# Kernel optimization log

Measured on AMD Instinct MI355X. Metric: run time of the kernel, lower is better.

Reference implementation:

```python
import jax, jax.numpy as jnp
import numpy as np
import math

ATTN_C = 32
HEADS = 8
IN_C = 256
PAIR_C = 128
B, M, N = 1, 128, 256


def _layernorm(x, w, b, eps=1e-5):
    mu = jnp.mean(x, axis=-1, keepdims=True)
    xc = x - mu
    var = jnp.mean(xc * xc, axis=-1, keepdims=True)
    return xc * jax.lax.rsqrt(var + eps) * w + b


def setup_inputs() -> dict:
    key = jax.random.key(0)
    ks = jax.random.split(key, 10)
    s1 = 1.0 / math.sqrt(IN_C)
    s2 = 1.0 / math.sqrt(PAIR_C)
    s3 = 1.0 / math.sqrt(ATTN_C * HEADS)
    return {
        "x1d": jax.random.normal(ks[0], (B, M, N, IN_C), jnp.float32),
        "x2d": jax.random.normal(ks[1], (B, N, N, PAIR_C), jnp.float32),
        "norm_w": jnp.ones((IN_C,), jnp.float32),
        "norm_b": jnp.zeros((IN_C,), jnp.float32),
        "qkv_w": jax.random.normal(ks[2], (3 * ATTN_C * HEADS, IN_C), jnp.float32) * s1,
        "x2d_w": jax.random.normal(ks[3], (HEADS, PAIR_C), jnp.float32) * s2,
        "gate_w": jax.random.normal(ks[4], (ATTN_C * HEADS, IN_C), jnp.float32) * s1,
        "gate_b": jnp.zeros((ATTN_C * HEADS,), jnp.float32),
        "final_w": jax.random.normal(ks[5], (IN_C, ATTN_C * HEADS), jnp.float32) * s3,
        "final_b": jnp.zeros((IN_C,), jnp.float32),
    }


def reference(x1d, x2d, norm_w, norm_b, qkv_w, x2d_w, gate_w, gate_b, final_w, final_b):
    c, h = ATTN_C, HEADS
    x = _layernorm(x1d, norm_w, norm_b)                      # [B,M,N,IN_C]
    qkv = (x @ qkv_w.T).reshape(*x.shape[:-1], c, 3 * h)     # [B,M,N,c,3h]
    q, k, v = qkv[..., :h], qkv[..., h:2 * h], qkv[..., 2 * h:]
    aff = jnp.einsum('bmich,bmjch->bmijh', q, k)             # [B,M,N,N,H]
    gate = jax.nn.sigmoid(x @ gate_w.T + gate_b).reshape(*x.shape[:-1], c, h)
    factor = 1.0 / math.sqrt(c)
    bias = (x2d @ x2d_w.T) * factor                          # [B,N,N,H]
    weights = jax.nn.softmax(aff + bias[:, None], axis=-2)   # softmax over j
    out = jnp.einsum('bmrch,bmirh->bmich', v, weights) * gate
    out = out.reshape(*x.shape[:-1], c * h) @ final_w.T + final_b
    return out
```

## Files before the change

kernel.cpp:

```cpp
#include <hip/hip_runtime.h>
#include <math.h>

typedef short bf16x8 __attribute__((ext_vector_type(8)));
typedef float f32x4  __attribute__((ext_vector_type(4)));

#define NPOS 32768

#define OFF_CHI   0u
#define OFF_AHI   100663296u
#define OFF_ATTN  134217728u
#define OFF_BIAST 150994944u
#define OFF_WHI   153354240u
#define OFF_W2P   154402816u
#define OFF_GBP   154533888u

__device__ __forceinline__ short f2bf(float x) {
    unsigned int u = __float_as_uint(x);
    unsigned int r = (u + 0x7FFFu + ((u >> 16) & 1u)) >> 16;
    return (short)r;
}
__device__ __forceinline__ float bf2f(short s) {
    return __uint_as_float(((unsigned int)(unsigned short)s) << 16);
}
__device__ __forceinline__ void async_copy16(const void* g, void* l) {
    __builtin_amdgcn_global_load_lds(
        (const __attribute__((address_space(1))) unsigned int*)g,
        (__attribute__((address_space(3))) unsigned int*)l, 16, 0, 0);
}

__global__ void k_ln_cast(const float* __restrict__ x,
                          const float* __restrict__ nw, const float* __restrict__ nb,
                          short* __restrict__ Ahi) {
    int wid = (blockIdx.x * blockDim.x + threadIdx.x) >> 6;
    int lane = threadIdx.x & 63;
    const float4 v = ((const float4*)(x + (size_t)wid * 256))[lane];
    float s  = v.x + v.y + v.z + v.w;
    float ss = v.x*v.x + v.y*v.y + v.z*v.z + v.w*v.w;
    #pragma unroll
    for (int o = 32; o; o >>= 1) {
        s  += __shfl_xor(s,  o, 64);
        ss += __shfl_xor(ss, o, 64);
    }
    float mu  = s * (1.0f / 256);
    float var = ss * (1.0f / 256) - mu * mu;
    float rs  = rsqrtf(var + 1e-5f);
    const float4 wv = ((const float4*)nw)[lane];
    const float4 bv = ((const float4*)nb)[lane];
    float y[4] = {(v.x - mu) * rs * wv.x + bv.x, (v.y - mu) * rs * wv.y + bv.y,
                  (v.z - mu) * rs * wv.z + bv.z, (v.w - mu) * rs * wv.w + bv.w};
    short h4[4];
    #pragma unroll
    for (int i = 0; i < 4; ++i) h4[i] = f2bf(y[i]);
    *(short4*)(Ahi + (size_t)wid * 256 + lane * 4) = *(short4*)h4;
}

__global__ void k_castw(const float* __restrict__ qkvw, const float* __restrict__ gatew,
                        const float* __restrict__ gateb, const float* __restrict__ finalw,
                        short* __restrict__ Whi, short* __restrict__ W2p,
                        float* __restrict__ gbp) {
    int r = blockIdx.x, t = threadIdx.x;
    if (r < 1024) {
        int which = r >> 8, h = (r >> 5) & 7, c = r & 31;
        const float* src = (which < 3) ? qkvw + (size_t)(c * 24 + which * 8 + h) * 256
                                       : gatew + (size_t)(c * 8 + h) * 256;
        Whi[(size_t)r * 256 + t] = f2bf(src[t]);
    } else if (r < 1280) {
        int o = r - 1024;
        int h = t >> 5, c = t & 31;
        W2p[(size_t)o * 256 + t] = f2bf(finalw[(size_t)o * 256 + c * 8 + h]);
    } else {
        int h = t >> 5, c = t & 31;
        gbp[t] = gateb[c * 8 + h];
    }
}

__global__ __launch_bounds__(256) void k_bias2(const float* __restrict__ x2d,
                                               const float* __restrict__ x2dw,
                                               float* __restrict__ biasT) {
    __shared__ float xs[64][132];
    __shared__ float ws[8][132];
    const int t = threadIdx.x;
    const int wid0 = blockIdx.x * 64;
    #pragma unroll
    for (int r = 0; r < 8; ++r) {
        int g = r * 256 + t;
        int row = g >> 5, c4 = g & 31;
        float4 v = *(const float4*)(x2d + (size_t)(wid0 + row) * 128 + c4 * 4);
        *(float4*)&xs[row][c4 * 4] = v;
    }
    {
        int h = t >> 5, c4 = t & 31;
        *(float4*)&ws[h][c4 * 4] = *(const float4*)(x2dw + h * 128 + c4 * 4);
    }
    __syncthreads();
    const float f = 0.17677669529663687f;
    const int i = wid0 >> 8;
    #pragma unroll
    for (int kk = 0; kk < 2; ++kk) {
        int o = t + kk * 256;
        int row = o >> 3, h = o & 7;
        float acc = 0.f;
        #pragma unroll
        for (int c4 = 0; c4 < 32; ++c4) {
            float4 xv = *(const float4*)&xs[row][c4 * 4];
            float4 wv = *(const float4*)&ws[h][c4 * 4];
            acc += xv.x * wv.x + xv.y * wv.y + xv.z * wv.z + xv.w * wv.w;
        }
        int j = (wid0 & 255) + row;
        biasT[(((h * 256 + j)) << 8) + i] = acc * f;
    }
}

__global__ __launch_bounds__(256) void k_gemm1m(
    const short* __restrict__ Ahi, const short* __restrict__ Whi,
    const float* __restrict__ gbp, short* __restrict__ Chi) {
    __shared__ short As[128 * 64];
    __shared__ short Bs[128 * 64];
    const int t = threadIdx.x;
    const int wave = t >> 6, lane = t & 63, ln15 = lane & 15, quad = lane >> 4;
    const int posBase = blockIdx.x * 128;
    const int nb = blockIdx.y;
    const int i0w = (wave & 1) * 64, n0w = (wave >> 1) * 64;

    f32x4 acc[4][4];
    #pragma unroll
    for (int a = 0; a < 4; ++a)
        #pragma unroll
        for (int b = 0; b < 4; ++b) acc[a][b] = (f32x4){0.f, 0.f, 0.f, 0.f};

    for (int k0 = 0; k0 < 256; k0 += 64) {
        #pragma unroll
        for (int r = 0; r < 4; ++r) {
            int g = r * 256 + t;
            int row = g >> 3, cs = g & 7;
            int colg = cs ^ (row & 7);
            size_t aoff = (size_t)(posBase + row) * 256 + k0 + colg * 8;
            size_t boff = (size_t)(nb * 128 + row) * 256 + k0 + colg * 8;
            int ldst = (r * 256 + wave * 64) * 8;
            async_copy16(Ahi + aoff, &As[ldst]);
            async_copy16(Whi + boff, &Bs[ldst]);
        }
        __syncthreads();
        #pragma unroll
        for (int kc = 0; kc < 2; ++kc) {
            bf16x8 af[4], bfr[4];
            #pragma unroll
            for (int it = 0; it < 4; ++it) {
                int rowa = i0w + it * 16 + ln15;
                int c8a = (kc * 4 + quad) ^ (rowa & 7);
                af[it] = *(const bf16x8*)&As[rowa * 64 + c8a * 8];
                int rowb = n0w + it * 16 + ln15;
                int c8b = (kc * 4 + quad) ^ (rowb & 7);
                bfr[it] = *(const bf16x8*)&Bs[rowb * 64 + c8b * 8];
            }
            #pragma unroll
            for (int it = 0; it < 4; ++it)
                #pragma unroll
                for (int nt = 0; nt < 4; ++nt)
                    acc[it][nt] = __builtin_amdgcn_mfma_f32_16x16x32_bf16(
                        af[it], bfr[nt], acc[it][nt], 0, 0, 0);
        }
        __syncthreads();
    }
    const bool isgate = (nb >= 6);
    #pragma unroll
    for (int it = 0; it < 4; ++it)
        #pragma unroll
        for (int nt = 0; nt < 4; ++nt)
            #pragma unroll
            for (int r = 0; r < 4; ++r) {
                size_t pos = posBase + i0w + it * 16 + quad * 4 + r;
                int ncol = nb * 128 + n0w + nt * 16 + ln15;
                float val = acc[it][nt][r];
                if (isgate) val = 1.0f / (1.0f + __expf(-(val + gbp[ncol - 768])));
                Chi[pos * 1024 + ncol] = f2bf(val);
            }
}

__global__ __launch_bounds__(512) void k_attn3(
    const short* __restrict__ Chi, const float* __restrict__ biasT,
    short* __restrict__ attnB) {
    __shared__ short Khi[256 * 32];
    __shared__ short VT[32 * 264];
    __shared__ short Pl[8][16][40];

    const int mh = blockIdx.x;
    const int m = mh >> 3, h = mh & 7;
    const int t = threadIdx.x;
    const int wave = t >> 6, lane = t & 63, ln15 = lane & 15, quad = lane >> 4;
    const int i0 = wave * 32;

    #pragma unroll
    for (int r = 0; r < 2; ++r) {
        int g = r * 512 + t;
        int j = g >> 2, c16 = g & 3;
        int cs = c16 ^ (j & 3);
        const short* gp = Chi + (size_t)(m * 256 + j) * 1024 + 256 + h * 32 + cs * 8;
        async_copy16(gp, &Khi[(r * 512 + wave * 64) * 8]);
    }
    {
        int j = t & 255, c0 = (t >> 8) * 16;
        const short* vp = Chi + (size_t)(m * 256 + j) * 1024 + 512 + h * 32 + c0;
        bf16x8 v0 = *(const bf16x8*)vp;
        bf16x8 v1 = *(const bf16x8*)(vp + 8);
        #pragma unroll
        for (int c = 0; c < 8; ++c) VT[(c0 + c) * 264 + j] = v0[c];
        #pragma unroll
        for (int c = 0; c < 8; ++c) VT[(c0 + 8 + c) * 264 + j] = v1[c];
    }
    bf16x8 qhi[2];
    #pragma unroll
    for (int it = 0; it < 2; ++it) {
        int i = i0 + it * 16 + ln15;
        qhi[it] = *(const bf16x8*)(Chi + (size_t)(m * 256 + i) * 1024 + h * 32 + quad * 8);
    }
    __syncthreads();

    float lacc[2] = {0.f, 0.f};
    f32x4 Oacc[2][2];
    #pragma unroll
    for (int a = 0; a < 2; ++a) {
        Oacc[a][0] = (f32x4){0.f, 0.f, 0.f, 0.f};
        Oacc[a][1] = (f32x4){0.f, 0.f, 0.f, 0.f};
    }
    const float* bp = biasT + (size_t)h * 65536;

    for (int j0 = 0; j0 < 256; j0 += 32) {
        bf16x8 kfh[2], vf[2];
        #pragma unroll
        for (int jt = 0; jt < 2; ++jt) {
            int j = j0 + jt * 16 + ln15;
            int cs = quad ^ (j & 3);
            kfh[jt] = *(const bf16x8*)&Khi[j * 32 + cs * 8];
        }
        #pragma unroll
        for (int ct = 0; ct < 2; ++ct) {
            int c = ct * 16 + ln15;
            vf[ct] = *(const bf16x8*)&VT[c * 264 + j0 + quad * 8];
        }
        #pragma unroll
        for (int it = 0; it < 2; ++it) {
            int i = i0 + it * 16 + ln15;
            float b0[4], b1[4];
            #pragma unroll
            for (int r = 0; r < 4; ++r) {
                b0[r] = bp[(j0 + quad * 4 + r) * 256 + i];
                b1[r] = bp[(j0 + 16 + quad * 4 + r) * 256 + i];
            }
            f32x4 s0 = (f32x4){0.f, 0.f, 0.f, 0.f};
            f32x4 s1 = (f32x4){0.f, 0.f, 0.f, 0.f};
            s0 = __builtin_amdgcn_mfma_f32_16x16x32_bf16(kfh[0], qhi[it], s0, 0, 0, 0);
            s1 = __builtin_amdgcn_mfma_f32_16x16x32_bf16(kfh[1], qhi[it], s1, 0, 0, 0);
            float p[8], ps = 0.f;
            #pragma unroll
            for (int r = 0; r < 4; ++r) { p[r] = __expf(s0[r] + b0[r]); ps += p[r]; }
            #pragma unroll
            for (int r = 0; r < 4; ++r) { p[4 + r] = __expf(s1[r] + b1[r]); ps += p[4 + r]; }
            lacc[it] += ps;
            unsigned long long pw0 =
                  (unsigned long long)(unsigned short)f2bf(p[0])
                | ((unsigned long long)(unsigned short)f2bf(p[1]) << 16)
                | ((unsigned long long)(unsigned short)f2bf(p[2]) << 32)
                | ((unsigned long long)(unsigned short)f2bf(p[3]) << 48);
            unsigned long long pw1 =
                  (unsigned long long)(unsigned short)f2bf(p[4])
                | ((unsigned long long)(unsigned short)f2bf(p[5]) << 16)
                | ((unsigned long long)(unsigned short)f2bf(p[6]) << 32)
                | ((unsigned long long)(unsigned short)f2bf(p[7]) << 48);
            *(unsigned long long*)&Pl[wave][ln15][quad * 4]      = pw0;
            *(unsigned long long*)&Pl[wave][ln15][16 + quad * 4] = pw1;
            bf16x8 pf = *(const bf16x8*)&Pl[wave][ln15][quad * 8];
            Oacc[it][0] = __builtin_amdgcn_mfma_f32_16x16x32_bf16(pf, vf[0], Oacc[it][0], 0, 0, 0);
            Oacc[it][1] = __builtin_amdgcn_mfma_f32_16x16x32_bf16(pf, vf[1], Oacc[it][1], 0, 0, 0);
        }
    }
    #pragma unroll
    for (int it = 0; it < 2; ++it) {
        float l = lacc[it];
        l += __shfl_xor(l, 16, 64);
        l += __shfl_xor(l, 32, 64);
        float inv = 1.0f / l;
        float invr[4];
        #pragma unroll
        for (int r = 0; r < 4; ++r) invr[r] = __shfl(inv, quad * 4 + r, 16);
        #pragma unroll
        for (int ct = 0; ct < 2; ++ct) {
            int c = ct * 16 + ln15;
            #pragma unroll
            for (int r = 0; r < 4; ++r) {
                int i = i0 + it * 16 + quad * 4 + r;
                float g = bf2f(Chi[(size_t)(m * 256 + i) * 1024 + 768 + h * 32 + c]);
                float val = Oacc[it][ct][r] * invr[r] * g;
                attnB[(size_t)(m * 256 + i) * 256 + h * 32 + c] = f2bf(val);
            }
        }
    }
}

__global__ __launch_bounds__(256) void k_gemm2m(
    const short* __restrict__ A, const short* __restrict__ W2p,
    const float* __restrict__ fb, float* __restrict__ out) {
    __shared__ short As[128 * 64];
    __shared__ short Bs[128 * 64];
    const int t = threadIdx.x;
    const int wave = t >> 6, lane = t & 63, ln15 = lane & 15, quad = lane >> 4;
    const int posBase = blockIdx.x * 128;
    const int nb = blockIdx.y;
    const int i0w = (wave & 1) * 64, n0w = (wave >> 1) * 64;

    f32x4 acc[4][4];
    #pragma unroll
    for (int a = 0; a < 4; ++a)
        #pragma unroll
        for (int b = 0; b < 4; ++b) acc[a][b] = (f32x4){0.f, 0.f, 0.f, 0.f};

    for (int k0 = 0; k0 < 256; k0 += 64) {
        #pragma unroll
        for (int r = 0; r < 4; ++r) {
            int g = r * 256 + t;
            int row = g >> 3, cs = g & 7;
            int colg = cs ^ (row & 7);
            const short* ga = A + (size_t)(posBase + row) * 256 + k0 + colg * 8;
            async_copy16(ga, &As[(r * 256 + wave * 64) * 8]);
            const short* gb = W2p + (size_t)(nb * 128 + row) * 256 + k0 + colg * 8;
            async_copy16(gb, &Bs[(r * 256 + wave * 64) * 8]);
        }
        __syncthreads();
        #pragma unroll
        for (int kc = 0; kc < 2; ++kc) {
            bf16x8 af[4], bfr[4];
            #pragma unroll
            for (int it = 0; it < 4; ++it) {
                int rowa = i0w + it * 16 + ln15;
                int c8a = (kc * 4 + quad) ^ (rowa & 7);
                af[it] = *(const bf16x8*)&As[rowa * 64 + c8a * 8];
                int rowb = n0w + it * 16 + ln15;
                int c8b = (kc * 4 + quad) ^ (rowb & 7);
                bfr[it] = *(const bf16x8*)&Bs[rowb * 64 + c8b * 8];
            }
            #pragma unroll
            for (int it = 0; it < 4; ++it)
                #pragma unroll
                for (int nt = 0; nt < 4; ++nt)
                    acc[it][nt] = __builtin_amdgcn_mfma_f32_16x16x32_bf16(
                        af[it], bfr[nt], acc[it][nt], 0, 0, 0);
        }
        __syncthreads();
    }
    #pragma unroll
    for (int it = 0; it < 4; ++it)
        #pragma unroll
        for (int nt = 0; nt < 4; ++nt)
            #pragma unroll
            for (int r = 0; r < 4; ++r) {
                size_t pos = posBase + i0w + it * 16 + quad * 4 + r;
                int ncol = nb * 128 + n0w + nt * 16 + ln15;
                out[pos * 256 + ncol] = acc[it][nt][r] + fb[ncol];
            }
}

extern "C" void kernel_launch(void* const* d_in, const int* in_sizes, int n_in,
                              void* d_out, int out_size, void* d_ws, size_t ws_size,
                              hipStream_t stream) {
    const float* x1d     = (const float*)d_in[0];
    const float* x2d     = (const float*)d_in[1];
    const float* norm_w  = (const float*)d_in[2];
    const float* norm_b  = (const float*)d_in[3];
    const float* qkv_w   = (const float*)d_in[4];
    const float* x2d_w   = (const float*)d_in[5];
    const float* gate_w  = (const float*)d_in[6];
    const float* gate_b  = (const float*)d_in[7];
    const float* final_w = (const float*)d_in[8];
    const float* final_b = (const float*)d_in[9];
    float* out = (float*)d_out;
    char* w = (char*)d_ws;

    short* Chi   = (short*)(w + OFF_CHI);
    short* Ahi   = (short*)(w + OFF_AHI);
    short* attnB = (short*)(w + OFF_ATTN);
    float* biasT = (float*)(w + OFF_BIAST);
    short* Whi   = (short*)(w + OFF_WHI);
    short* W2p   = (short*)(w + OFF_W2P);
    float* gbp   = (float*)(w + OFF_GBP);

    k_ln_cast<<<NPOS / 4, 256, 0, stream>>>(x1d, norm_w, norm_b, Ahi);
    k_castw<<<1281, 256, 0, stream>>>(qkv_w, gate_w, gate_b, final_w, Whi, W2p, gbp);
    k_bias2<<<1024, 256, 0, stream>>>(x2d, x2d_w, biasT);
    k_gemm1m<<<dim3(256, 8), 256, 0, stream>>>(Ahi, Whi, gbp, Chi);
    k_attn3<<<1024, 512, 0, stream>>>(Chi, biasT, attnB);
    k_gemm2m<<<dim3(256, 2), 256, 0, stream>>>(attnB, W2p, final_b, out);
}
```

Baseline: 224.2 us.

## Double-buffer GEMM tiles, transpose bias layout, and use exp2 with packed bf16 converts

Both GEMM kernels now double-buffer their LDS A/B tiles, issuing the next k-slice's async copies before computing the current one, so global loads overlap MFMA work. The bias kernel writes bias in [h][i][j] order with the log2(e) factor folded in. This lets the attention kernel read it as contiguous float4 instead of eight strided scalar loads. The attention kernel computes exp2 via fma and packs probabilities with v_cvt_pk_bf16_f32, and the K LDS swizzle gains an extra XOR term to reduce bank conflicts. Doubling LDS per GEMM block may lower occupancy. The unsynchronized prefetch depends on the async copy wait semantics, which are not visible here.

After: 244.5 us. +9.1%, slower.

```diff
diff --git a/kernel.cpp b/kernel.cpp
--- a/kernel.cpp
+++ b/kernel.cpp
@@ -5,6 +5,7 @@
 typedef float f32x4  __attribute__((ext_vector_type(4)));
 
 #define NPOS 32768
+#define LOG2E 1.4426950408889634f
 
 #define OFF_CHI   0u
 #define OFF_AHI   100663296u
@@ -93,12 +94,11 @@
         *(float4*)&ws[h][c4 * 4] = *(const float4*)(x2dw + h * 128 + c4 * 4);
     }
     __syncthreads();
-    const float f = 0.17677669529663687f;
-    const int i = wid0 >> 8;
+    const float f = 0.17677669529663687f * LOG2E;
     #pragma unroll
     for (int kk = 0; kk < 2; ++kk) {
         int o = t + kk * 256;
-        int row = o >> 3, h = o & 7;
+        int h = o >> 6, row = o & 63;
         float acc = 0.f;
         #pragma unroll
         for (int c4 = 0; c4 < 32; ++c4) {
@@ -106,16 +106,15 @@
             float4 wv = *(const float4*)&ws[h][c4 * 4];
             acc += xv.x * wv.x + xv.y * wv.y + xv.z * wv.z + xv.w * wv.w;
         }
-        int j = (wid0 & 255) + row;
-        biasT[(((h * 256 + j)) << 8) + i] = acc * f;
+        biasT[((size_t)h << 16) + wid0 + row] = acc * f;
     }
 }
 
 __global__ __launch_bounds__(256) void k_gemm1m(
     const short* __restrict__ Ahi, const short* __restrict__ Whi,
     const float* __restrict__ gbp, short* __restrict__ Chi) {
-    __shared__ short As[128 * 64];
-    __shared__ short Bs[128 * 64];
+    __shared__ short As[2][128 * 64];
+    __shared__ short Bs[2][128 * 64];
     const int t = threadIdx.x;
     const int wave = t >> 6, lane = t & 63, ln15 = lane & 15, quad = lane >> 4;
     const int posBase = blockIdx.x * 128;
@@ -128,7 +127,7 @@
         #pragma unroll
         for (int b = 0; b < 4; ++b) acc[a][b] = (f32x4){0.f, 0.f, 0.f, 0.f};
 
-    for (int k0 = 0; k0 < 256; k0 += 64) {
+    auto stage = [&](int buf, int k0) {
         #pragma unroll
         for (int r = 0; r < 4; ++r) {
             int g = r * 256 + t;
@@ -137,10 +136,16 @@
             size_t aoff = (size_t)(posBase + row) * 256 + k0 + colg * 8;
             size_t boff = (size_t)(nb * 128 + row) * 256 + k0 + colg * 8;
             int ldst = (r * 256 + wave * 64) * 8;
-            async_copy16(Ahi + aoff, &As[ldst]);
-            async_copy16(Whi + boff, &Bs[ldst]);
-        }
-        __syncthreads();
+            async_copy16(Ahi + aoff, &As[buf][ldst]);
+            async_copy16(Whi + boff, &Bs[buf][ldst]);
+        }
+    };
+    stage(0, 0);
+    __syncthreads();
+    #pragma unroll
+    for (int ks = 0; ks < 4; ++ks) {
+        const int cur = ks & 1;
+        if (ks < 3) stage(cur ^ 1, (ks + 1) * 64);
         #pragma unroll
         for (int kc = 0; kc < 2; ++kc) {
             bf16x8 af[4], bfr[4];
@@ -148,10 +153,10 @@
             for (int it = 0; it < 4; ++it) {
                 int rowa = i0w + it * 16 + ln15;
                 int c8a = (kc * 4 + quad) ^ (rowa & 7);
-                af[it] = *(const bf16x8*)&As[rowa * 64 + c8a * 8];
+                af[it] = *(const bf16x8*)&As[cur][rowa * 64 + c8a * 8];
                 int rowb = n0w + it * 16 + ln15;
                 int c8b = (kc * 4 + quad) ^ (rowb & 7);
-                bfr[it] = *(const bf16x8*)&Bs[rowb * 64 + c8b * 8];
+                bfr[it] = *(const bf16x8*)&Bs[cur][rowb * 64 + c8b * 8];
             }
             #pragma unroll
             for (int it = 0; it < 4; ++it)
@@ -160,7 +165,7 @@
                     acc[it][nt] = __builtin_amdgcn_mfma_f32_16x16x32_bf16(
                         af[it], bfr[nt], acc[it][nt], 0, 0, 0);
         }
-        __syncthreads();
+        if (ks < 3) __syncthreads();
     }
     const bool isgate = (nb >= 6);
     #pragma unroll
@@ -194,7 +199,7 @@
     for (int r = 0; r < 2; ++r) {
         int g = r * 512 + t;
         int j = g >> 2, c16 = g & 3;
-        int cs = c16 ^ (j & 3);
+        int cs = c16 ^ (j & 3) ^ ((j >> 2) & 3);
         const short* gp = Chi + (size_t)(m * 256 + j) * 1024 + 256 + h * 32 + cs * 8;
         async_copy16(gp, &Khi[(r * 512 + wave * 64) * 8]);
     }
@@ -230,7 +235,7 @@
         #pragma unroll
         for (int jt = 0; jt < 2; ++jt) {
             int j = j0 + jt * 16 + ln15;
-            int cs = quad ^ (j & 3);
+            int cs = quad ^ (j & 3) ^ ((j >> 2) & 3);
             kfh[jt] = *(const bf16x8*)&Khi[j * 32 + cs * 8];
         }
         #pragma unroll
@@ -241,34 +246,28 @@
         #pragma unroll
         for (int it = 0; it < 2; ++it) {
             int i = i0 + it * 16 + ln15;
-            float b0[4], b1[4];
-            #pragma unroll
-            for (int r = 0; r < 4; ++r) {
-                b0[r] = bp[(j0 + quad * 4 + r) * 256 + i];
-                b1[r] = bp[(j0 + 16 + quad * 4 + r) * 256 + i];
-            }
+            const float4 bv0 = *(const float4*)&bp[(size_t)i * 256 + j0 + quad * 4];
+            const float4 bv1 = *(const float4*)&bp[(size_t)i * 256 + j0 + 16 + quad * 4];
             f32x4 s0 = (f32x4){0.f, 0.f, 0.f, 0.f};
             f32x4 s1 = (f32x4){0.f, 0.f, 0.f, 0.f};
             s0 = __builtin_amdgcn_mfma_f32_16x16x32_bf16(kfh[0], qhi[it], s0, 0, 0, 0);
             s1 = __builtin_amdgcn_mfma_f32_16x16x32_bf16(kfh[1], qhi[it], s1, 0, 0, 0);
-            float p[8], ps = 0.f;
-            #pragma unroll
-            for (int r = 0; r < 4; ++r) { p[r] = __expf(s0[r] + b0[r]); ps += p[r]; }
-            #pragma unroll
-            for (int r = 0; r < 4; ++r) { p[4 + r] = __expf(s1[r] + b1[r]); ps += p[4 + r]; }
-            lacc[it] += ps;
-            unsigned long long pw0 =
-                  (unsigned long long)(unsigned short)f2bf(p[0])
-                | ((unsigned long long)(unsigned short)f2bf(p[1]) << 16)
-                | ((unsigned long long)(unsigned short)f2bf(p[2]) << 32)
-                | ((unsigned long long)(unsigned short)f2bf(p[3]) << 48);
-            unsigned long long pw1 =
-                  (unsigned long long)(unsigned short)f2bf(p[4])
-                | ((unsigned long long)(unsigned short)f2bf(p[5]) << 16)
-                | ((unsigned long long)(unsigned short)f2bf(p[6]) << 32)
-                | ((unsigned long long)(unsigned short)f2bf(p[7]) << 48);
-            *(unsigned long long*)&Pl[wave][ln15][quad * 4]      = pw0;
-            *(unsigned long long*)&Pl[wave][ln15][16 + quad * 4] = pw1;
+            float p0 = __builtin_amdgcn_exp2f(fmaf(s0[0], LOG2E, bv0.x));
+            float p1 = __builtin_amdgcn_exp2f(fmaf(s0[1], LOG2E, bv0.y));
+            float p2 = __builtin_amdgcn_exp2f(fmaf(s0[2], LOG2E, bv0.z));
+            float p3 = __builtin_amdgcn_exp2f(fmaf(s0[3], LOG2E, bv0.w));
+            float p4 = __builtin_amdgcn_exp2f(fmaf(s1[0], LOG2E, bv1.x));
+            float p5 = __builtin_amdgcn_exp2f(fmaf(s1[1], LOG2E, bv1.y));
+            float p6 = __builtin_amdgcn_exp2f(fmaf(s1[2], LOG2E, bv1.z));
+            float p7 = __builtin_amdgcn_exp2f(fmaf(s1[3], LOG2E, bv1.w));
+            lacc[it] += ((p0 + p1) + (p2 + p3)) + ((p4 + p5) + (p6 + p7));
+            unsigned u01, u23, u45, u67;
+            asm("v_cvt_pk_bf16_f32 %0, %1, %2" : "=v"(u01) : "v"(p0), "v"(p1));
+            asm("v_cvt_pk_bf16_f32 %0, %1, %2" : "=v"(u23) : "v"(p2), "v"(p3));
+            asm("v_cvt_pk_bf16_f32 %0, %1, %2" : "=v"(u45) : "v"(p4), "v"(p5));
+            asm("v_cvt_pk_bf16_f32 %0, %1, %2" : "=v"(u67) : "v"(p6), "v"(p7));
+            *(uint2*)&Pl[wave][ln15][quad * 4]      = make_uint2(u01, u23);
+            *(uint2*)&Pl[wave][ln15][16 + quad * 4] = make_uint2(u45, u67);
             bf16x8 pf = *(const bf16x8*)&Pl[wave][ln15][quad * 8];
             Oacc[it][0] = __builtin_amdgcn_mfma_f32_16x16x32_bf16(pf, vf[0], Oacc[it][0], 0, 0, 0);
             Oacc[it][1] = __builtin_amdgcn_mfma_f32_16x16x32_bf16(pf, vf[1], Oacc[it][1], 0, 0, 0);
@@ -300,8 +299,8 @@
 __global__ __launch_bounds__(256) void k_gemm2m(
     const short* __restrict__ A, const short* __restrict__ W2p,
     const float* __restrict__ fb, float* __restrict__ out) {
-    __shared__ short As[128 * 64];
-    __shared__ short Bs[128 * 64];
+    __shared__ short As[2][128 * 64];
+    __shared__ short Bs[2][128 * 64];
     const int t = threadIdx.x;
     const int wave = t >> 6, lane = t & 63, ln15 = lane & 15, quad = lane >> 4;
     const int posBase = blockIdx.x * 128;
@@ -314,18 +313,25 @@
         #pragma unroll
         for (int b = 0; b < 4; ++b) acc[a][b] = (f32x4){0.f, 0.f, 0.f, 0.f};
 
-    for (int k0 = 0; k0 < 256; k0 += 64) {
+    auto stage = [&](int buf, int k0) {
         #pragma unroll
         for (int r = 0; r < 4; ++r) {
             int g = r * 256 + t;
             int row = g >> 3, cs = g & 7;
             int colg = cs ^ (row & 7);
-            const short* ga = A + (size_t)(posBase + row) * 256 + k0 + colg * 8;
-            async_copy16(ga, &As[(r * 256 + wave * 64) * 8]);
-            const short* gb = W2p + (size_t)(nb * 128 + row) * 256 + k0 + colg * 8;
-            async_copy16(gb, &Bs[(r * 256 + wave * 64) * 8]);
-        }
-        __syncthreads();
+            size_t aoff = (size_t)(posBase + row) * 256 + k0 + colg * 8;
+            size_t boff = (size_t)(nb * 128 + row) * 256 + k0 + colg * 8;
+            int ldst = (r * 256 + wave * 64) * 8;
+            async_copy16(A + aoff, &As[buf][ldst]);
+            async_copy16(W2p + boff, &Bs[buf][ldst]);
+        }
+    };
+    stage(0, 0);
+    __syncthreads();
+    #pragma unroll
+    for (int ks = 0; ks < 4; ++ks) {
+        const int cur = ks & 1;
+        if (ks < 3) stage(cur ^ 1, (ks + 1) * 64);
         #pragma unroll
         for (int kc = 0; kc < 2; ++kc) {
             bf16x8 af[4], bfr[4];
@@ -333,10 +339,10 @@
             for (int it = 0; it < 4; ++it) {
                 int rowa = i0w + it * 16 + ln15;
                 int c8a = (kc * 4 + quad) ^ (rowa & 7);
-                af[it] = *(const bf16x8*)&As[rowa * 64 + c8a * 8];
+                af[it] = *(const bf16x8*)&As[cur][rowa * 64 + c8a * 8];
                 int rowb = n0w + it * 16 + ln15;
                 int c8b = (kc * 4 + quad) ^ (rowb & 7);
-                bfr[it] = *(const bf16x8*)&Bs[rowb * 64 + c8b * 8];
+                bfr[it] = *(const bf16x8*)&Bs[cur][rowb * 64 + c8b * 8];
             }
             #pragma unroll
             for (int it = 0; it < 4; ++it)
@@ -345,7 +351,7 @@
                     acc[it][nt] = __builtin_amdgcn_mfma_f32_16x16x32_bf16(
                         af[it], bfr[nt], acc[it][nt], 0, 0, 0);
         }
-        __syncthreads();
+        if (ks < 3) __syncthreads();
     }
     #pragma unroll
     for (int it = 0; it < 4; ++it)
```
